# Optimization experiments

Hardware: AMD Instinct MI355X
Metric: run time of the kernel (lower is better)

Reference implementation:

```python
import jax, jax.numpy as jnp
import numpy as np

POS_IN, HID, DIR_IN, SIG_OUT, COL_OUT = 63, 128, 27, 1, 3
TOTAL = POS_IN * HID + HID + HID * SIG_OUT + SIG_OUT + (HID + DIR_IN) * COL_OUT + COL_OUT  # 8717
B, N = 32, 65536


def positional_encoding(x, num_freqs):
    # x: [..., D] -> [..., D + D*2*num_freqs]
    freqs = 2.0 ** jnp.arange(num_freqs, dtype=x.dtype)  # [F]
    x_exp = x[..., None] * freqs                          # [..., D, F]
    flat = x_exp.reshape(*x.shape[:-1], -1)               # [..., D*F]
    return jnp.concatenate([x, jnp.sin(flat), jnp.cos(flat)], axis=-1)


def setup_inputs() -> dict:
    key = jax.random.key(0)
    k1, k2, k3 = jax.random.split(key, 3)
    params = jax.random.normal(k1, (B, TOTAL), dtype=jnp.float32) * 0.1
    points = jax.random.uniform(k2, (B, N, 3), dtype=jnp.float32, minval=-1.0, maxval=1.0)
    dirs = jax.random.uniform(k3, (B, N, 3), dtype=jnp.float32, minval=-1.0, maxval=1.0)
    return {"params": params, "points": points, "dirs": dirs}


def _unpack(params):
    b = params.shape[0]
    i = 0
    pw = params[:, i:i + POS_IN * HID].reshape(b, HID, POS_IN); i += POS_IN * HID
    pb = params[:, i:i + HID]; i += HID
    sw = params[:, i:i + HID * SIG_OUT].reshape(b, SIG_OUT, HID); i += HID * SIG_OUT
    sb = params[:, i:i + SIG_OUT]; i += SIG_OUT
    cin = HID + DIR_IN
    cw = params[:, i:i + cin * COL_OUT].reshape(b, COL_OUT, cin); i += cin * COL_OUT
    cb = params[:, i:i + COL_OUT]
    return pw, pb, sw, sb, cw, cb


def reference(params, points, dirs):
    pw, pb, sw, sb, cw, cb = _unpack(params)
    pos_enc = positional_encoding(points, 10)   # [B,N,63]
    dir_enc = positional_encoding(dirs, 4)      # [B,N,27]
    h = jnp.einsum('bni,bhi->bnh', pos_enc, pw) + pb[:, None, :]  # [B,N,128]
    h = jax.nn.relu(h)
    sigma = jnp.einsum('bnh,boh->bno', h, sw) + sb[:, None, :]    # [B,N,1]
    h_dir = jnp.concatenate([h, dir_enc], axis=-1)                # [B,N,155]
    color = jnp.einsum('bnc,boc->bno', h_dir, cw) + cb[:, None, :]  # [B,N,3]
    color = jax.nn.sigmoid(color)
    return jnp.concatenate([color, sigma], axis=-1)               # [B,N,4]
```

## Files before the change

### kernel.cpp

```cpp
#include <hip/hip_runtime.h>

#define POS_IN 63
#define HID 128
#define TOTAL 8789
#define NB 32
#define NPTS 65536

#define PB_OFF 8064
#define SW_OFF 8192
#define SB_OFF 8320
#define CW_OFF 8321
#define CB_OFF 8786

#define BLOCKS_PER_BATCH 16
#define PTS_PER_BLOCK (NPTS / BLOCKS_PER_BATCH)
#define ITERS (PTS_PER_BLOCK / 256)

typedef __attribute__((ext_vector_type(8))) short s16x8;
typedef __attribute__((ext_vector_type(4))) float f32x4;
typedef __bf16 bf16x2 __attribute__((ext_vector_type(2)));

__device__ __forceinline__ unsigned short f2bf(float v) {
    unsigned u = __builtin_bit_cast(unsigned, v);
    unsigned r = 0x7fffu + ((u >> 16) & 1u);
    return (unsigned short)((u + r) >> 16);
}
__device__ __forceinline__ unsigned pk2(float a, float b) {
    bf16x2 v;
    v[0] = (__bf16)a;
    v[1] = (__bf16)b;
    return __builtin_bit_cast(unsigned, v);
}

__global__ __launch_bounds__(256) void nerf_mlp_kernel(
        const float* __restrict__ params,
        const float* __restrict__ points,
        const float* __restrict__ dirs,
        float* __restrict__ out)
{
    __shared__ __align__(16) unsigned char smem[49152];
    unsigned short* stage = (unsigned short*)smem;

    const int tid = threadIdx.x;
    const int lane = tid & 63;
    const int wid = tid >> 6;
    const int b = blockIdx.y;
    const float* P = params + (size_t)b * TOTAL;

    for (int idx = tid; idx < 8064; idx += 256) {
        int n = idx / 63;
        int k = idx - n * 63;
        stage[n * 72 + k] = f2bf(P[idx]);
        if (k == 0) stage[n * 72 + 63] = f2bf(P[PB_OFF + n]);
    }
    __syncthreads();

    const int c = lane & 15;
    const int kg = lane >> 4;

    s16x8 wB[8][2];
    #pragma unroll
    for (int nt = 0; nt < 8; ++nt) {
        #pragma unroll
        for (int kh = 0; kh < 2; ++kh) {
            int n = nt * 16 + c;
            int k = kh * 32 + kg * 8;
            uint4 raw = *(const uint4*)&stage[n * 72 + k];
            wB[nt][kh] = __builtin_bit_cast(s16x8, raw);
        }
    }

    s16x8 wB2h[4];
    #pragma unroll
    for (int m = 0; m < 4; ++m) {
        uint4 dd = make_uint4(0u, 0u, 0u, 0u);
        if (c < 4) {
            const int base = (c == 3) ? SW_OFF : (CW_OFF + c * 155);
            const int b0 = base + 32 * m + kg * 4;
            dd.x = pk2(P[b0 + 0],  P[b0 + 1]);
            dd.y = pk2(P[b0 + 2],  P[b0 + 3]);
            dd.z = pk2(P[b0 + 16], P[b0 + 17]);
            dd.w = pk2(P[b0 + 18], P[b0 + 19]);
        }
        wB2h[m] = __builtin_bit_cast(s16x8, dd);
    }
    s16x8 wB2d;
    {
        float vals[8];
        #pragma unroll
        for (int e = 0; e < 8; ++e) {
            int k_loc = kg * 8 + e;
            float v = 0.f;
            if (c < 3) {
                if (k_loc < 27)       v = P[CW_OFF + c * 155 + 128 + k_loc];
                else if (k_loc == 27) v = P[CB_OFF + c];
            } else if (c == 3) {
                if (k_loc == 27)      v = P[SB_OFF];
            }
            vals[e] = v;
        }
        uint4 dd;
        dd.x = pk2(vals[0], vals[1]);
        dd.y = pk2(vals[2], vals[3]);
        dd.z = pk2(vals[4], vals[5]);
        dd.w = pk2(vals[6], vals[7]);
        wB2d = __builtin_bit_cast(s16x8, dd);
    }
    __syncthreads();

    unsigned char* encb = smem + wid * 8192;
    unsigned char* dirb = smem + 32768 + wid * 4096;

    const size_t bpts = (size_t)b * NPTS;
    const int n0b = blockIdx.x * PTS_PER_BLOCK;

    for (int it = 0; it < ITERS; ++it) {
        const int n0 = n0b + it * 256 + wid * 64;
        const int p = n0 + lane;

        const float* pp = points + (bpts + p) * 3;
        float x = pp[0], y = pp[1], z = pp[2];
        const float* dd = dirs + (bpts + p) * 3;
        float dx = dd[0], dy = dd[1], dz = dd[2];

        float d[32];
        d[0] = dx; d[1] = dy; d[2] = dz;
        d[27] = 1.0f; d[28] = 0.f; d[29] = 0.f; d[30] = 0.f; d[31] = 0.f;
        #pragma unroll
        for (int i = 0; i < 3; ++i) {
            float v = (i == 0) ? dx : (i == 1) ? dy : dz;
            float s = __sinf(v), co = __cosf(v);
            d[3 + i * 4] = s; d[15 + i * 4] = co;
            #pragma unroll
            for (int f = 1; f < 4; ++f) {
                float ns = 2.f * s * co;
                float nc = 1.f - 2.f * s * s;
                s = ns; co = nc;
                d[3 + i * 4 + f] = s;
                d[15 + i * 4 + f] = co;
            }
        }
        #pragma unroll
        for (int kq = 0; kq < 4; ++kq) {
            uint4 q;
            q.x = pk2(d[kq * 8 + 0], d[kq * 8 + 1]);
            q.y = pk2(d[kq * 8 + 2], d[kq * 8 + 3]);
            q.z = pk2(d[kq * 8 + 4], d[kq * 8 + 5]);
            q.w = pk2(d[kq * 8 + 6], d[kq * 8 + 7]);
            *(uint4*)(dirb + kq * 1024 + lane * 16) = q;
        }

        float e[64];
        e[0] = x; e[1] = y; e[2] = z; e[63] = 1.0f;
        #pragma unroll
        for (int i = 0; i < 3; ++i) {
            float v = (i == 0) ? x : (i == 1) ? y : z;
            float s = __sinf(v), co = __cosf(v);
            e[3 + i * 10] = s; e[33 + i * 10] = co;
            #pragma unroll
            for (int f = 1; f < 10; ++f) {
                float ns = 2.f * s * co;
                float nc = 1.f - 2.f * s * s;
                s = ns; co = nc;
                e[3 + i * 10 + f] = s;
                e[33 + i * 10 + f] = co;
            }
        }
        #pragma unroll
        for (int kq = 0; kq < 8; ++kq) {
            uint4 q;
            q.x = pk2(e[kq * 8 + 0], e[kq * 8 + 1]);
            q.y = pk2(e[kq * 8 + 2], e[kq * 8 + 3]);
            q.z = pk2(e[kq * 8 + 4], e[kq * 8 + 5]);
            q.w = pk2(e[kq * 8 + 6], e[kq * 8 + 7]);
            *(uint4*)(encb + kq * 1024 + lane * 16) = q;
        }

        float* outp = out + (bpts + n0) * 4;

        #pragma unroll
        for (int t = 0; t < 4; ++t) {
            uint4 a0r = *(const uint4*)(encb + kg * 1024 + (t * 16 + c) * 16);
            uint4 a1r = *(const uint4*)(encb + (4 + kg) * 1024 + (t * 16 + c) * 16);
            s16x8 A0 = __builtin_bit_cast(s16x8, a0r);
            s16x8 A1 = __builtin_bit_cast(s16x8, a1r);

            uint4 adr = *(const uint4*)(dirb + kg * 1024 + (t * 16 + c) * 16);
            s16x8 A2d = __builtin_bit_cast(s16x8, adr);
            f32x4 acc2 = (f32x4){0.f, 0.f, 0.f, 0.f};
            acc2 = __builtin_amdgcn_mfma_f32_16x16x32_bf16(A2d, wB2d, acc2, 0, 0, 0);

            #pragma unroll
            for (int m = 0; m < 4; ++m) {
                f32x4 accA = (f32x4){0.f, 0.f, 0.f, 0.f};
                f32x4 accB = (f32x4){0.f, 0.f, 0.f, 0.f};
                accA = __builtin_amdgcn_mfma_f32_16x16x32_bf16(wB[2 * m][0], A0, accA, 0, 0, 0);
                accA = __builtin_amdgcn_mfma_f32_16x16x32_bf16(wB[2 * m][1], A1, accA, 0, 0, 0);
                accB = __builtin_amdgcn_mfma_f32_16x16x32_bf16(wB[2 * m + 1][0], A0, accB, 0, 0, 0);
                accB = __builtin_amdgcn_mfma_f32_16x16x32_bf16(wB[2 * m + 1][1], A1, accB, 0, 0, 0);
                uint4 dd2;
                dd2.x = pk2(fmaxf(accA[0], 0.f), fmaxf(accA[1], 0.f));
                dd2.y = pk2(fmaxf(accA[2], 0.f), fmaxf(accA[3], 0.f));
                dd2.z = pk2(fmaxf(accB[0], 0.f), fmaxf(accB[1], 0.f));
                dd2.w = pk2(fmaxf(accB[2], 0.f), fmaxf(accB[3], 0.f));
                s16x8 A2 = __builtin_bit_cast(s16x8, dd2);
                acc2 = __builtin_amdgcn_mfma_f32_16x16x32_bf16(A2, wB2h[m], acc2, 0, 0, 0);
            }

            if (c < 4) {
                #pragma unroll
                for (int j = 0; j < 4; ++j) {
                    float v = acc2[j];
                    float sig = 1.f / (1.f + __expf(-v));
                    v = (c < 3) ? sig : v;
                    outp[t * 64 + kg * 16 + j * 4 + c] = v;
                }
            }
        }
    }
}

extern "C" void kernel_launch(void* const* d_in, const int* in_sizes, int n_in,
                              void* d_out, int out_size, void* d_ws, size_t ws_size,
                              hipStream_t stream) {
    const float* params = (const float*)d_in[0];
    const float* points = (const float*)d_in[1];
    const float* dirs   = (const float*)d_in[2];
    float* out = (float*)d_out;
    dim3 grid(BLOCKS_PER_BATCH, NB);
    nerf_mlp_kernel<<<grid, 256, 0, stream>>>(params, points, dirs, out);
}
```

Measured before the change: 98.29 us.

## Compute direction color term with scalar FMAs, use 512-thread blocks, split accumulators

Replaces the direction-encoding MFMA, which went through LDS staging, with per-lane scalar FMAs. These compute the three color contributions directly from the params, and the results are passed through a small LDS buffer. Blocks grow to 8 waves with 72KB of shared memory. The second-layer accumulation is split into two chains to shorten MFMA dependency latency. The scalar path adds VALU work and repeated global param loads per point, and the larger blocks may reduce occupancy.

```diff
diff --git a/kernel.cpp b/kernel.cpp
--- a/kernel.cpp
+++ b/kernel.cpp
@@ -12,9 +12,11 @@
 #define CW_OFF 8321
 #define CB_OFF 8786
 
+#define THREADS 512
+#define WAVES 8
 #define BLOCKS_PER_BATCH 16
 #define PTS_PER_BLOCK (NPTS / BLOCKS_PER_BATCH)
-#define ITERS (PTS_PER_BLOCK / 256)
+#define ITERS (PTS_PER_BLOCK / (WAVES * 64))
 
 typedef __attribute__((ext_vector_type(8))) short s16x8;
 typedef __attribute__((ext_vector_type(4))) float f32x4;
@@ -32,13 +34,13 @@
     return __builtin_bit_cast(unsigned, v);
 }
 
-__global__ __launch_bounds__(256) void nerf_mlp_kernel(
+__global__ __launch_bounds__(THREADS) void nerf_mlp_kernel(
         const float* __restrict__ params,
         const float* __restrict__ points,
         const float* __restrict__ dirs,
         float* __restrict__ out)
 {
-    __shared__ __align__(16) unsigned char smem[49152];
+    __shared__ __align__(16) unsigned char smem[73728];
     unsigned short* stage = (unsigned short*)smem;
 
     const int tid = threadIdx.x;
@@ -47,7 +49,7 @@
     const int b = blockIdx.y;
     const float* P = params + (size_t)b * TOTAL;
 
-    for (int idx = tid; idx < 8064; idx += 256) {
+    for (int idx = tid; idx < 8064; idx += THREADS) {
         int n = idx / 63;
         int k = idx - n * 63;
         stage[n * 72 + k] = f2bf(P[idx]);
@@ -84,38 +86,18 @@
         }
         wB2h[m] = __builtin_bit_cast(s16x8, dd);
     }
-    s16x8 wB2d;
-    {
-        float vals[8];
-        #pragma unroll
-        for (int e = 0; e < 8; ++e) {
-            int k_loc = kg * 8 + e;
-            float v = 0.f;
-            if (c < 3) {
-                if (k_loc < 27)       v = P[CW_OFF + c * 155 + 128 + k_loc];
-                else if (k_loc == 27) v = P[CB_OFF + c];
-            } else if (c == 3) {
-                if (k_loc == 27)      v = P[SB_OFF];
-            }
-            vals[e] = v;
-        }
-        uint4 dd;
-        dd.x = pk2(vals[0], vals[1]);
-        dd.y = pk2(vals[2], vals[3]);
-        dd.z = pk2(vals[4], vals[5]);
-        dd.w = pk2(vals[6], vals[7]);
-        wB2d = __builtin_bit_cast(s16x8, dd);
-    }
+    const float cbias = P[c < 3 ? (CB_OFF + c) : SB_OFF];
+
     __syncthreads();
 
     unsigned char* encb = smem + wid * 8192;
-    unsigned char* dirb = smem + 32768 + wid * 4096;
+    float* cpb = (float*)(smem + 65536 + wid * 1024);
 
     const size_t bpts = (size_t)b * NPTS;
     const int n0b = blockIdx.x * PTS_PER_BLOCK;
 
     for (int it = 0; it < ITERS; ++it) {
-        const int n0 = n0b + it * 256 + wid * 64;
+        const int n0 = n0b + it * (WAVES * 64) + wid * 64;
         const int p = n0 + lane;
 
         const float* pp = points + (bpts + p) * 3;
@@ -123,32 +105,32 @@
         const float* dd = dirs + (bpts + p) * 3;
         float dx = dd[0], dy = dd[1], dz = dd[2];
 
-        float d[32];
-        d[0] = dx; d[1] = dy; d[2] = dz;
-        d[27] = 1.0f; d[28] = 0.f; d[29] = 0.f; d[30] = 0.f; d[31] = 0.f;
+        float cp0 = 0.f, cp1 = 0.f, cp2 = 0.f;
         #pragma unroll
         for (int i = 0; i < 3; ++i) {
             float v = (i == 0) ? dx : (i == 1) ? dy : dz;
+            cp0 = fmaf(v, P[CW_OFF + 128 + i], cp0);
+            cp1 = fmaf(v, P[CW_OFF + 155 + 128 + i], cp1);
+            cp2 = fmaf(v, P[CW_OFF + 310 + 128 + i], cp2);
             float s = __sinf(v), co = __cosf(v);
-            d[3 + i * 4] = s; d[15 + i * 4] = co;
             #pragma unroll
-            for (int f = 1; f < 4; ++f) {
-                float ns = 2.f * s * co;
-                float nc = 1.f - 2.f * s * s;
-                s = ns; co = nc;
-                d[3 + i * 4 + f] = s;
-                d[15 + i * 4 + f] = co;
-            }
-        }
-        #pragma unroll
-        for (int kq = 0; kq < 4; ++kq) {
-            uint4 q;
-            q.x = pk2(d[kq * 8 + 0], d[kq * 8 + 1]);
-            q.y = pk2(d[kq * 8 + 2], d[kq * 8 + 3]);
-            q.z = pk2(d[kq * 8 + 4], d[kq * 8 + 5]);
-            q.w = pk2(d[kq * 8 + 6], d[kq * 8 + 7]);
-            *(uint4*)(dirb + kq * 1024 + lane * 16) = q;
-        }
+            for (int f = 0; f < 4; ++f) {
+                if (f > 0) {
+                    float ns = 2.f * s * co;
+                    float nc = 1.f - 2.f * s * s;
+                    s = ns; co = nc;
+                }
+                int si = 128 + 3 + i * 4 + f;
+                int ci = 128 + 15 + i * 4 + f;
+                cp0 = fmaf(s, P[CW_OFF + si], cp0);
+                cp1 = fmaf(s, P[CW_OFF + 155 + si], cp1);
+                cp2 = fmaf(s, P[CW_OFF + 310 + si], cp2);
+                cp0 = fmaf(co, P[CW_OFF + ci], cp0);
+                cp1 = fmaf(co, P[CW_OFF + 155 + ci], cp1);
+                cp2 = fmaf(co, P[CW_OFF + 310 + ci], cp2);
+            }
+        }
+        *(float4*)(cpb + lane * 4) = make_float4(cp0, cp1, cp2, 0.f);
 
         float e[64];
         e[0] = x; e[1] = y; e[2] = z; e[63] = 1.0f;
@@ -185,11 +167,8 @@
             s16x8 A0 = __builtin_bit_cast(s16x8, a0r);
             s16x8 A1 = __builtin_bit_cast(s16x8, a1r);
 
-            uint4 adr = *(const uint4*)(dirb + kg * 1024 + (t * 16 + c) * 16);
-            s16x8 A2d = __builtin_bit_cast(s16x8, adr);
-            f32x4 acc2 = (f32x4){0.f, 0.f, 0.f, 0.f};
-            acc2 = __builtin_amdgcn_mfma_f32_16x16x32_bf16(A2d, wB2d, acc2, 0, 0, 0);
-
+            f32x4 acc2a = (f32x4){0.f, 0.f, 0.f, 0.f};
+            f32x4 acc2b = (f32x4){0.f, 0.f, 0.f, 0.f};
             #pragma unroll
             for (int m = 0; m < 4; ++m) {
                 f32x4 accA = (f32x4){0.f, 0.f, 0.f, 0.f};
@@ -204,13 +183,18 @@
                 dd2.z = pk2(fmaxf(accB[0], 0.f), fmaxf(accB[1], 0.f));
                 dd2.w = pk2(fmaxf(accB[2], 0.f), fmaxf(accB[3], 0.f));
                 s16x8 A2 = __builtin_bit_cast(s16x8, dd2);
-                acc2 = __builtin_amdgcn_mfma_f32_16x16x32_bf16(A2, wB2h[m], acc2, 0, 0, 0);
+                if (m & 1)
+                    acc2b = __builtin_amdgcn_mfma_f32_16x16x32_bf16(A2, wB2h[m], acc2b, 0, 0, 0);
+                else
+                    acc2a = __builtin_amdgcn_mfma_f32_16x16x32_bf16(A2, wB2h[m], acc2a, 0, 0, 0);
             }
 
             if (c < 4) {
                 #pragma unroll
                 for (int j = 0; j < 4; ++j) {
-                    float v = acc2[j];
+                    int pt = t * 16 + kg * 4 + j;
+                    float v = acc2a[j] + acc2b[j] + cbias;
+                    if (c < 3) v += cpb[pt * 4 + c];
                     float sig = 1.f / (1.f + __expf(-v));
                     v = (c < 3) ? sig : v;
                     outp[t * 64 + kg * 16 + j * 4 + c] = v;
@@ -228,5 +212,5 @@
     const float* dirs   = (const float*)d_in[2];
     float* out = (float*)d_out;
     dim3 grid(BLOCKS_PER_BATCH, NB);
-    nerf_mlp_kernel<<<grid, 256, 0, stream>>>(params, points, dirs, out);
-}
+    nerf_mlp_kernel<<<grid, THREADS, 0, stream>>>(params, points, dirs, out);
+}
```

After: 104.0 us. +5.8%, slower.
